# Kernel optimization log

Hardware: AMD Instinct MI355X
Metric: run time of the kernel (lower is better)

Reference implementation:

```python
import jax, jax.numpy as jnp
import numpy as np

N_NODES = 100000


def sage_conv(x, src, dst, W_l, b_l, W_r, n_nodes):
    # mean-aggregate source neighbors onto destination nodes (PyG SAGEConv, aggr='mean')
    agg = jax.ops.segment_sum(x[src], dst, num_segments=n_nodes)          # [N, d_in]
    cnt = jax.ops.segment_sum(jnp.ones((src.shape[0], 1), x.dtype), dst,
                              num_segments=n_nodes)                        # [N, 1]
    agg = agg / jnp.maximum(cnt, 1.0)  # isolated nodes -> 0, as in scatter-mean
    # out = lin_l(agg) + lin_r(x); bias lives in lin_l
    return agg @ W_l + b_l + x @ W_r


def setup_inputs() -> dict:
    key = jax.random.key(0)
    ks = jax.random.split(key, 12)
    d_in, h1, h2, h3 = 256, 256, 128, 1
    x = jax.random.normal(ks[0], (N_NODES, d_in), dtype=jnp.float32)
    edge_index = jax.random.randint(ks[1], (2, 1600000), 0, N_NODES, dtype=jnp.int64)

    def lin(k, din, dout):
        s = 1.0 / np.sqrt(din)
        return jax.random.uniform(k, (din, dout), jnp.float32, -s, s)

    return {
        "x": x,
        "edge_index": edge_index,
        "Wl1": lin(ks[2], d_in, h1), "bl1": jnp.zeros((h1,), jnp.float32), "Wr1": lin(ks[3], d_in, h1),
        "Wl2": lin(ks[4], h1, h2),  "bl2": jnp.zeros((h2,), jnp.float32), "Wr2": lin(ks[5], h1, h2),
        "Wl3": lin(ks[6], h2, h3),  "bl3": jnp.zeros((h3,), jnp.float32), "Wr3": lin(ks[7], h2, h3),
    }


def reference(x, edge_index, Wl1, bl1, Wr1, Wl2, bl2, Wr2, Wl3, bl3, Wr3):
    src, dst = edge_index[0], edge_index[1]
    n = x.shape[0]
    h = jax.nn.relu(sage_conv(x, src, dst, Wl1, bl1, Wr1, n))
    h = jax.nn.relu(sage_conv(h, src, dst, Wl2, bl2, Wr2, n))
    out = sage_conv(h, src, dst, Wl3, bl3, Wr3, n)
    return out  # [N, 1]
```

## Files before the change

kernel.cpp:

```cpp
#include <hip/hip_runtime.h>
#include <hip/hip_bf16.h>


typedef __attribute__((ext_vector_type(8))) short short8;
typedef __attribute__((ext_vector_type(4))) float f32x4;

__device__ __forceinline__ unsigned short f2b(float f) {
    __hip_bfloat16 h = __float2bfloat16(f);
    return *reinterpret_cast<unsigned short*>(&h);
}
__device__ __forceinline__ float b2f(unsigned short u) {
    union { unsigned int i; float f; } v; v.i = ((unsigned int)u) << 16; return v.f;
}
__device__ __forceinline__ unsigned char f2q(float f) {
    unsigned int p = __builtin_amdgcn_cvt_pk_fp8_f32(f, f, 0u, false);
    return (unsigned char)(p & 0xffu);
}

__device__ __forceinline__ void gload_lds16(const unsigned short* g, unsigned short* l) {
    __builtin_amdgcn_global_load_lds(
        (const __attribute__((address_space(1))) unsigned int*)(const void*)g,
        (__attribute__((address_space(3))) unsigned int*)(void*)l,
        16, 0, 0);
}

__device__ __forceinline__ void acc_fp8x8(const uint2 v, float* s) {
    s[0] += __builtin_amdgcn_cvt_f32_fp8(v.x, 0);
    s[1] += __builtin_amdgcn_cvt_f32_fp8(v.x, 1);
    s[2] += __builtin_amdgcn_cvt_f32_fp8(v.x, 2);
    s[3] += __builtin_amdgcn_cvt_f32_fp8(v.x, 3);
    s[4] += __builtin_amdgcn_cvt_f32_fp8(v.y, 0);
    s[5] += __builtin_amdgcn_cvt_f32_fp8(v.y, 1);
    s[6] += __builtin_amdgcn_cvt_f32_fp8(v.y, 2);
    s[7] += __builtin_amdgcn_cvt_f32_fp8(v.y, 3);
}

__global__ __launch_bounds__(256) void prep_fused(
    const float* __restrict__ x, unsigned short* __restrict__ xb,
    const float* __restrict__ Wl1, const float* __restrict__ Wr1,
    const float* __restrict__ Wl2, const float* __restrict__ Wr2,
    unsigned short* __restrict__ Wl1s, unsigned short* __restrict__ Wr1s,
    unsigned short* __restrict__ Wl2s, unsigned short* __restrict__ Wr2s,
    const int* __restrict__ dst, int* __restrict__ deg,
    unsigned short* __restrict__ rank, int E)
{
    const int b = blockIdx.x;
    const int tid = threadIdx.x;
    if (b < 25000) {
        const int i = b * 256 + tid;
        float4 v = *(const float4*)(x + (size_t)i * 4);
        ushort4 o;
        o.x = f2b(v.x); o.y = f2b(v.y); o.z = f2b(v.z); o.w = f2b(v.w);
        *(ushort4*)(xb + (size_t)i * 4) = o;
        if (tid < 64) {
            const int e = b * 64 + tid;
            if (e < E) rank[e] = (unsigned short)atomicAdd(&deg[dst[e]], 1);
        }
    } else {
        const float* W; unsigned short* O; int base, hs;
        if (b < 25256)      { W = Wl1; O = Wl1s; base = b - 25000; hs = 8; }
        else if (b < 25512) { W = Wr1; O = Wr1s; base = b - 25256; hs = 8; }
        else if (b < 25640) { W = Wl2; O = Wl2s; base = b - 25512; hs = 7; }
        else                { W = Wr2; O = Wr2s; base = b - 25640; hs = 7; }
        const int i = base * 256 + tid;
        const int k = i >> hs;
        const int h = i & ((1 << hs) - 1);
        O[((size_t)(((k >> 3) << hs) + h) << 3) + (k & 7)] = f2b(W[i]);
    }
}

__global__ __launch_bounds__(256) void scan_phaseA(int* __restrict__ a,
                                                   int* __restrict__ blockSums, int n) {
    __shared__ int sh[256];
    const int tid = threadIdx.x;
    const int base = blockIdx.x * 1024 + tid * 4;
    int v[4];
    #pragma unroll
    for (int i = 0; i < 4; ++i) v[i] = (base + i < n) ? a[base + i] : 0;
    int tsum = v[0] + v[1] + v[2] + v[3];
    sh[tid] = tsum;
    __syncthreads();
    for (int off = 1; off < 256; off <<= 1) {
        int t = (tid >= off) ? sh[tid - off] : 0;
        __syncthreads();
        sh[tid] += t;
        __syncthreads();
    }
    int run = sh[tid] - tsum;
    #pragma unroll
    for (int i = 0; i < 4; ++i) {
        if (base + i < n) a[base + i] = run;
        run += v[i];
    }
    if (tid == 255) blockSums[blockIdx.x] = sh[255];
}

__global__ __launch_bounds__(256) void scan_phaseB(int* __restrict__ bs, int nb) {
    __shared__ int sh[256];
    const int tid = threadIdx.x;
    int v = (tid < nb) ? bs[tid] : 0;
    sh[tid] = v;
    __syncthreads();
    for (int off = 1; off < 256; off <<= 1) {
        int t = (tid >= off) ? sh[tid - off] : 0;
        __syncthreads();
        sh[tid] += t;
        __syncthreads();
    }
    if (tid < nb) bs[tid] = sh[tid] - v;
}

__global__ __launch_bounds__(256) void scan_phaseC(int* __restrict__ a,
                                                   const int* __restrict__ bs, int n) {
    const int base = blockIdx.x * 1024 + threadIdx.x * 4;
    const int add = bs[blockIdx.x];
    #pragma unroll
    for (int i = 0; i < 4; ++i)
        if (base + i < n) a[base + i] += add;
}

__global__ __launch_bounds__(256) void gemm_l1_fill(
    const unsigned short* __restrict__ Xb,
    const unsigned short* __restrict__ Wsw_l,
    const unsigned short* __restrict__ Wsw_r,
    const float* __restrict__ bias,
    unsigned char* __restrict__ Tout,
    unsigned short* __restrict__ Abase,
    int M,
    const int* __restrict__ src, const int* __restrict__ dst,
    const int* __restrict__ starts, const unsigned short* __restrict__ rank,
    int* __restrict__ csr, int E)
{
    const int bid = (blockIdx.x & 7) * 1173 + (blockIdx.x >> 3);
    const int grp = bid / 3;
    const int rem = bid - grp * 3;
    const int tid = threadIdx.x;

    if (rem != 0) {
        const int e = (grp * 2 + rem - 1) * 256 + tid;
        if (e < E) csr[starts[dst[e]] + (int)rank[e]] = src[e];
        return;
    }

    __shared__ unsigned short smem[16384];

    const int wid = tid >> 6;
    const int lane = tid & 63;
    const int quad = lane >> 4;
    const int l15 = lane & 15;
    const int col0 = (grp & 3) << 6;
    const int m0 = (grp >> 2) * 128;

    const unsigned short* aSrc[4];
    unsigned int aOfs[4];
    #pragma unroll
    for (int i = 0; i < 4; ++i) {
        const int slot = i * 256 + tid;
        const int r = slot >> 3, cs = slot & 7;
        const int cg = cs ^ (r & 7);
        aSrc[i] = Xb + ((size_t)(m0 + r) << 8) + (cg << 3);
        aOfs[i] = (unsigned)((i * 256 + wid * 64) * 8);
    }
    const unsigned short* bSrc[4];
    unsigned int bOfs[4];
    #pragma unroll
    for (int i = 0; i < 4; ++i) {
        const int slot = i * 256 + tid;
        const int mat = slot >> 9, ko = (slot >> 6) & 7, col = slot & 63;
        const unsigned short* Wm = mat ? Wsw_r : Wsw_l;
        bSrc[i] = Wm + (((size_t)ko * 256 + col0 + col) << 3);
        bOfs[i] = (unsigned)(8192 + (i * 256 + wid * 64) * 8);
    }

    const f32x4 zero = {0.f, 0.f, 0.f, 0.f};
    f32x4 acc[2][8];
    #pragma unroll
    for (int mt = 0; mt < 2; ++mt)
        #pragma unroll
        for (int nt = 0; nt < 8; ++nt) acc[mt][nt] = zero;

    for (int ks = 0; ks < 4; ++ks) {
        #pragma unroll
        for (int i = 0; i < 4; ++i)
            gload_lds16(aSrc[i] + ks * 64, smem + aOfs[i]);
        #pragma unroll
        for (int i = 0; i < 4; ++i)
            gload_lds16(bSrc[i] + ks * 16384, smem + bOfs[i]);
        __syncthreads();

        #pragma unroll
        for (int k32 = 0; k32 < 2; ++k32) {
            short8 af[2], bf[8];
            #pragma unroll
            for (int mt = 0; mt < 2; ++mt) {
                const int row = wid * 32 + mt * 16 + l15;
                const int c = (k32 * 4 + quad) ^ (row & 7);
                af[mt] = *(const short8*)(smem + ((row << 3) + c) * 8);
            }
            #pragma unroll
            for (int nt = 0; nt < 4; ++nt) {
                const int colL = nt * 16 + l15;
                const int ko = k32 * 4 + quad;
                bf[nt]     = *(const short8*)(smem + 8192 + ((ko << 6) + colL) * 8);
                bf[nt + 4] = *(const short8*)(smem + 8192 + (512 + (ko << 6) + colL) * 8);
            }
            #pragma unroll
            for (int mt = 0; mt < 2; ++mt)
                #pragma unroll
                for (int nt = 0; nt < 8; ++nt)
                    acc[mt][nt] = __builtin_amdgcn_mfma_f32_16x16x32_bf16(
                        af[mt], bf[nt], acc[mt][nt], 0, 0, 0);
        }
        __syncthreads();
    }

    #pragma unroll
    for (int nt = 0; nt < 4; ++nt) {
        const int colg = col0 + nt * 16 + l15;
        const float bb = bias[colg];
        #pragma unroll
        for (int mt = 0; mt < 2; ++mt) {
            const int gmb = m0 + wid * 32 + mt * 16 + quad * 4;
            #pragma unroll
            for (int r = 0; r < 4; ++r) {
                if (gmb + r < M) {
                    Tout [(size_t)(gmb + r) * 256 + colg] = f2q(acc[mt][nt][r]);
                    Abase[(size_t)(gmb + r) * 256 + colg] = f2b(acc[mt][nt + 4][r] + bb);
                }
            }
        }
    }
}

__global__ __launch_bounds__(256) void agg256_b(
    const int* __restrict__ endoff, const int* __restrict__ csr,
    const unsigned char* __restrict__ T,
    const unsigned short* __restrict__ Abase, unsigned short* __restrict__ Xout,
    int N, int E)
{
    const int node = (int)((blockIdx.x * 256 + threadIdx.x) >> 5);
    const int lane = threadIdx.x & 31;
    const int hsel = threadIdx.x & 32;
    if (node >= N) return;
    const int beg = endoff[node];
    const int end = (node + 1 < N) ? endoff[node + 1] : E;
    float s[8] = {0.f, 0.f, 0.f, 0.f, 0.f, 0.f, 0.f, 0.f};

    for (int base = beg; base < end; base += 32) {
        const int il = base + lane;
        const int vidx = csr[il < E ? il : (E - 1)];
        const int cnt = (end - base < 32) ? (end - base) : 32;
        int u = 0;
        for (; u + 16 <= cnt; u += 16) {
            uint2 v[16];
            #pragma unroll
            for (int k = 0; k < 16; ++k) {
                const int r = __shfl(vidx, (u + k) | hsel, 64);
                v[k] = *(const uint2*)(T + ((size_t)r << 8) + (lane << 3));
            }
            #pragma unroll
            for (int k = 0; k < 16; ++k) acc_fp8x8(v[k], s);
        }
        if (u + 8 <= cnt) {
            uint2 v[8];
            #pragma unroll
            for (int k = 0; k < 8; ++k) {
                const int r = __shfl(vidx, (u + k) | hsel, 64);
                v[k] = *(const uint2*)(T + ((size_t)r << 8) + (lane << 3));
            }
            #pragma unroll
            for (int k = 0; k < 8; ++k) acc_fp8x8(v[k], s);
            u += 8;
        }
        for (; u < cnt; ++u) {
            const int r = __shfl(vidx, u | hsel, 64);
            const uint2 v = *(const uint2*)(T + ((size_t)r << 8) + (lane << 3));
            acc_fp8x8(v, s);
        }
    }

    const float w = 1.0f / fmaxf((float)(end - beg), 1.0f);
    const short8 bu = *(const short8*)(Abase + ((size_t)node << 8) + (lane << 3));
    short8 o;
    #pragma unroll
    for (int j = 0; j < 8; ++j)
        o[j] = (short)f2b(fmaxf(b2f((unsigned short)bu[j]) + s[j] * w, 0.f));
    *(short8*)(Xout + ((size_t)node << 8) + (lane << 3)) = o;
}

__global__ __launch_bounds__(256) void gemm_bf16(
    const unsigned short* __restrict__ Xb,
    const unsigned short* __restrict__ Wsw_l,
    const unsigned short* __restrict__ Wsw_r,
    const float* __restrict__ bias,
    unsigned char* __restrict__ Tout,
    unsigned short* __restrict__ Abase,
    int M, int H)
{
    const int tid = threadIdx.x;
    const int wid = tid >> 6;
    const int lane = tid & 63;
    const int quad = lane >> 4;
    const int l15 = lane & 15;

    const int col0 = blockIdx.x << 6;
    const int m0 = blockIdx.y * 128 + wid * 32;

    const unsigned short* aptr[2];
    #pragma unroll
    for (int mt = 0; mt < 2; ++mt) {
        int r = m0 + mt * 16 + l15;
        if (r > M - 1) r = M - 1;
        aptr[mt] = Xb + ((size_t)r << 8) + (quad << 3);
    }
    const unsigned short* bptr[8];
    #pragma unroll
    for (int nt = 0; nt < 4; ++nt) {
        const int col = col0 + nt * 16 + l15;
        bptr[nt]     = Wsw_l + (((size_t)quad * H + col) << 3);
        bptr[nt + 4] = Wsw_r + (((size_t)quad * H + col) << 3);
    }

    const f32x4 zero = {0.f, 0.f, 0.f, 0.f};
    f32x4 acc[2][8];
    #pragma unroll
    for (int mt = 0; mt < 2; ++mt)
        #pragma unroll
        for (int nt = 0; nt < 8; ++nt) acc[mt][nt] = zero;

    #pragma unroll 2
    for (int ks = 0; ks < 8; ++ks) {
        short8 af[2], bf[8];
        #pragma unroll
        for (int mt = 0; mt < 2; ++mt)
            af[mt] = *(const short8*)(aptr[mt] + ks * 32);
        #pragma unroll
        for (int nt = 0; nt < 8; ++nt)
            bf[nt] = *(const short8*)(bptr[nt] + (size_t)ks * 32 * H);
        #pragma unroll
        for (int mt = 0; mt < 2; ++mt)
            #pragma unroll
            for (int nt = 0; nt < 8; ++nt)
                acc[mt][nt] = __builtin_amdgcn_mfma_f32_16x16x32_bf16(
                    af[mt], bf[nt], acc[mt][nt], 0, 0, 0);
    }

    #pragma unroll
    for (int nt = 0; nt < 4; ++nt) {
        const int colg = col0 + nt * 16 + l15;
        const float bb = bias[colg];
        #pragma unroll
        for (int mt = 0; mt < 2; ++mt) {
            const int gmb = m0 + mt * 16 + quad * 4;
            #pragma unroll
            for (int r = 0; r < 4; ++r) {
                if (gmb + r < M) {
                    Tout [(size_t)(gmb + r) * H + colg] = f2q(acc[mt][nt][r]);
                    Abase[(size_t)(gmb + r) * H + colg] = f2b(acc[mt][nt + 4][r] + bb);
                }
            }
        }
    }
}

__global__ __launch_bounds__(256) void agg_gemv3(
    const int* __restrict__ endoff, const int* __restrict__ csr,
    const unsigned char* __restrict__ T,
    const unsigned short* __restrict__ Ab,
    const float* __restrict__ Wl, const float* __restrict__ Wr,
    const float* __restrict__ b,
    float* __restrict__ t3, float* __restrict__ out, int N, int E)
{
    const int node = (int)((blockIdx.x * 256 + threadIdx.x) >> 5);
    const int lane = threadIdx.x & 31;
    const int hsel = threadIdx.x & 32;
    if (node >= N) return;
    const int beg = endoff[node];
    const int end = (node + 1 < N) ? endoff[node + 1] : E;
    float s0 = 0.f, s1 = 0.f, s2 = 0.f, s3 = 0.f;

    for (int base = beg; base < end; base += 32) {
        const int il = base + lane;
        const int vidx = csr[il < E ? il : (E - 1)];
        const int cnt = (end - base < 32) ? (end - base) : 32;
        int u = 0;
        for (; u + 16 <= cnt; u += 16) {
            unsigned int v[16];
            #pragma unroll
            for (int k = 0; k < 16; ++k) {
                const int r = __shfl(vidx, (u + k) | hsel, 64);
                v[k] = *(const unsigned int*)(T + ((size_t)r << 7) + (lane << 2));
            }
            #pragma unroll
            for (int k = 0; k < 16; ++k) {
                s0 += __builtin_amdgcn_cvt_f32_fp8(v[k], 0);
                s1 += __builtin_amdgcn_cvt_f32_fp8(v[k], 1);
                s2 += __builtin_amdgcn_cvt_f32_fp8(v[k], 2);
                s3 += __builtin_amdgcn_cvt_f32_fp8(v[k], 3);
            }
        }
        if (u + 8 <= cnt) {
            unsigned int v[8];
            #pragma unroll
            for (int k = 0; k < 8; ++k) {
                const int r = __shfl(vidx, (u + k) | hsel, 64);
                v[k] = *(const unsigned int*)(T + ((size_t)r << 7) + (lane << 2));
            }
            #pragma unroll
            for (int k = 0; k < 8; ++k) {
                s0 += __builtin_amdgcn_cvt_f32_fp8(v[k], 0);
                s1 += __builtin_amdgcn_cvt_f32_fp8(v[k], 1);
                s2 += __builtin_amdgcn_cvt_f32_fp8(v[k], 2);
                s3 += __builtin_amdgcn_cvt_f32_fp8(v[k], 3);
            }
            u += 8;
        }
        for (; u < cnt; ++u) {
            const int r = __shfl(vidx, u | hsel, 64);
            const unsigned int v = *(const unsigned int*)(T + ((size_t)r << 7) + (lane << 2));
            s0 += __builtin_amdgcn_cvt_f32_fp8(v, 0);
            s1 += __builtin_amdgcn_cvt_f32_fp8(v, 1);
            s2 += __builtin_amdgcn_cvt_f32_fp8(v, 2);
            s3 += __builtin_amdgcn_cvt_f32_fp8(v, 3);
        }
    }

    const float w = 1.0f / fmaxf((float)(end - beg), 1.0f);
    const ushort4 bu = *(const ushort4*)(Ab + ((size_t)node << 7) + (lane << 2));
    const float h0 = fmaxf(b2f(bu.x) + s0 * w, 0.f);
    const float h1 = fmaxf(b2f(bu.y) + s1 * w, 0.f);
    const float h2 = fmaxf(b2f(bu.z) + s2 * w, 0.f);
    const float h3 = fmaxf(b2f(bu.w) + s3 * w, 0.f);

    const float4 wl = *(const float4*)(Wl + (lane << 2));
    const float4 wr = *(const float4*)(Wr + (lane << 2));
    float dl = h0 * wl.x + h1 * wl.y + h2 * wl.z + h3 * wl.w;
    float dr = h0 * wr.x + h1 * wr.y + h2 * wr.z + h3 * wr.w;
    #pragma unroll
    for (int off = 16; off > 0; off >>= 1) {
        dl += __shfl_down(dl, off, 64);
        dr += __shfl_down(dr, off, 64);
    }
    if (lane == 0) {
        t3[node] = dl;
        out[node] = dr + b[0];
    }
}

__global__ __launch_bounds__(256) void agg1(
    const int* __restrict__ endoff, const int* __restrict__ csr,
    const float* __restrict__ t3, float* __restrict__ out, int N, int E)
{
    const int i = blockIdx.x * blockDim.x + threadIdx.x;
    if (i >= N) return;
    const int beg = endoff[i];
    const int end = (i + 1 < N) ? endoff[i + 1] : E;
    int p = beg;
    float s = 0.f;
    for (; p + 4 <= end; p += 4)
        s += (t3[csr[p]] + t3[csr[p + 1]]) + (t3[csr[p + 2]] + t3[csr[p + 3]]);
    for (; p < end; ++p) s += t3[csr[p]];
    out[i] += s / fmaxf((float)(end - beg), 1.0f);
}

extern "C" void kernel_launch(void* const* d_in, const int* in_sizes, int n_in,
                              void* d_out, int out_size, void* d_ws, size_t ws_size,
                              hipStream_t stream) {
    const float* x   = (const float*)d_in[0];
    const int*   ei  = (const int*)d_in[1];
    const float* Wl1 = (const float*)d_in[2];
    const float* bl1 = (const float*)d_in[3];
    const float* Wr1 = (const float*)d_in[4];
    const float* Wl2 = (const float*)d_in[5];
    const float* bl2 = (const float*)d_in[6];
    const float* Wr2 = (const float*)d_in[7];
    const float* Wl3 = (const float*)d_in[8];
    const float* bl3 = (const float*)d_in[9];
    const float* Wr3 = (const float*)d_in[10];
    float* out = (float*)d_out;

    const int N = in_sizes[0] / 256;
    const int E = in_sizes[1] / 2;
    const int* src = ei;
    const int* dst = ei + E;

    char* W = (char*)d_ws;
    const size_t MB512 = (size_t)100000 * 512;
    unsigned short* X1b = (unsigned short*)(W);
    unsigned char*  T1b = (unsigned char*)(W + MB512);
    unsigned short* A1b = (unsigned short*)(W + 2 * MB512);
    unsigned short* X2b = (unsigned short*)(W);
    unsigned char*  T2b = (unsigned char*)(W + MB512);
    unsigned short* A2b = (unsigned short*)(W + MB512 + MB512 / 2);
    char* S = W + 3 * MB512;
    int*   endoff = (int*)(S);
    int*   bsums  = (int*)(S + (size_t)N * 4);
    float* t3     = (float*)(S + (size_t)N * 4 + 1024);
    int*   csr    = (int*)(S + (size_t)N * 8 + 1024);
    unsigned short* Wl1s = (unsigned short*)(S + (size_t)N * 8 + 1024 + (size_t)E * 4);
    unsigned short* Wr1s = Wl1s + 65536;
    unsigned short* Wl2s = Wr1s + 65536;
    unsigned short* Wr2s = Wl2s + 32768;
    unsigned short* rank = Wr2s + 32768;

    hipMemsetAsync(endoff, 0, (size_t)N * sizeof(int), stream);
    prep_fused<<<25768, 256, 0, stream>>>(
        x, X1b, Wl1, Wr1, Wl2, Wr2, Wl1s, Wr1s, Wl2s, Wr2s,
        dst, endoff, rank, E);
    const int nScanBlocks = (N + 1023) / 1024;
    scan_phaseA<<<nScanBlocks, 256, 0, stream>>>(endoff, bsums, N);
    scan_phaseB<<<1, 256, 0, stream>>>(bsums, nScanBlocks);
    scan_phaseC<<<nScanBlocks, 256, 0, stream>>>(endoff, bsums, N);

    gemm_l1_fill<<<3128 * 3, 256, 0, stream>>>(X1b, Wl1s, Wr1s, bl1, T1b, A1b, N,
                                               src, dst, endoff, rank, csr, E);

    agg256_b<<<(N * 32 + 255) / 256, 256, 0, stream>>>(endoff, csr, T1b, A1b, X2b, N, E);
    gemm_bf16<<<dim3(2, (N + 127) / 128), 256, 0, stream>>>(X2b, Wl2s, Wr2s, bl2,
                                                            T2b, A2b, N, 128);

    agg_gemv3<<<(N * 32 + 255) / 256, 256, 0, stream>>>(endoff, csr, T2b, A2b,
                                                        Wl3, Wr3, bl3, t3, out, N, E);
    agg1<<<(N + 255) / 256, 256, 0, stream>>>(endoff, csr, t3, out, N, E);
}
```

Baseline: 482.1 us.

## Store layer-1 fp8 transform in column-sliced layout and aggregate per slice

The layer-1 GEMM now writes the fp8 transformed features as 8 column slices of 32 bytes per node, each slice contiguous over nodes. The aggregation kernel becomes agg256_s: each block handles one slice, and 4 lanes cover a node's 32-byte slice, so 16 nodes share a wave. The aim is a smaller per-slice gather working set that fits cache better. The cost is that each edge index is reread 8 times, and the per-node loop with one index per step gives less memory-level parallelism than the old shuffle-batched gathers.

```diff
diff --git a/kernel.cpp b/kernel.cpp
--- a/kernel.cpp
+++ b/kernel.cpp
@@ -218,13 +218,14 @@
     for (int nt = 0; nt < 4; ++nt) {
         const int colg = col0 + nt * 16 + l15;
         const float bb = bias[colg];
+        const size_t sbase = (size_t)(colg >> 5) * (size_t)M * 32 + (colg & 31);
         #pragma unroll
         for (int mt = 0; mt < 2; ++mt) {
             const int gmb = m0 + wid * 32 + mt * 16 + quad * 4;
             #pragma unroll
             for (int r = 0; r < 4; ++r) {
                 if (gmb + r < M) {
-                    Tout [(size_t)(gmb + r) * 256 + colg] = f2q(acc[mt][nt][r]);
+                    Tout [sbase + (size_t)(gmb + r) * 32] = f2q(acc[mt][nt][r]);
                     Abase[(size_t)(gmb + r) * 256 + colg] = f2b(acc[mt][nt + 4][r] + bb);
                 }
             }
@@ -232,60 +233,45 @@
     }
 }
 
-__global__ __launch_bounds__(256) void agg256_b(
+__global__ __launch_bounds__(256) void agg256_s(
     const int* __restrict__ endoff, const int* __restrict__ csr,
     const unsigned char* __restrict__ T,
     const unsigned short* __restrict__ Abase, unsigned short* __restrict__ Xout,
     int N, int E)
 {
-    const int node = (int)((blockIdx.x * 256 + threadIdx.x) >> 5);
-    const int lane = threadIdx.x & 31;
-    const int hsel = threadIdx.x & 32;
+    const int slice = blockIdx.x & 7;
+    const int lane  = threadIdx.x & 63;
+    const int g     = lane >> 2;
+    const int boff  = lane & 3;
+    const int node  = (blockIdx.x >> 3) * 64 + (threadIdx.x >> 6) * 16 + g;
     if (node >= N) return;
     const int beg = endoff[node];
     const int end = (node + 1 < N) ? endoff[node + 1] : E;
+    const unsigned char* Ts = T + (size_t)slice * (size_t)N * 32 + (boff << 3);
+
     float s[8] = {0.f, 0.f, 0.f, 0.f, 0.f, 0.f, 0.f, 0.f};
-
-    for (int base = beg; base < end; base += 32) {
-        const int il = base + lane;
-        const int vidx = csr[il < E ? il : (E - 1)];
-        const int cnt = (end - base < 32) ? (end - base) : 32;
-        int u = 0;
-        for (; u + 16 <= cnt; u += 16) {
-            uint2 v[16];
-            #pragma unroll
-            for (int k = 0; k < 16; ++k) {
-                const int r = __shfl(vidx, (u + k) | hsel, 64);
-                v[k] = *(const uint2*)(T + ((size_t)r << 8) + (lane << 3));
-            }
-            #pragma unroll
-            for (int k = 0; k < 16; ++k) acc_fp8x8(v[k], s);
-        }
-        if (u + 8 <= cnt) {
-            uint2 v[8];
-            #pragma unroll
-            for (int k = 0; k < 8; ++k) {
-                const int r = __shfl(vidx, (u + k) | hsel, 64);
-                v[k] = *(const uint2*)(T + ((size_t)r << 8) + (lane << 3));
-            }
-            #pragma unroll
-            for (int k = 0; k < 8; ++k) acc_fp8x8(v[k], s);
-            u += 8;
-        }
-        for (; u < cnt; ++u) {
-            const int r = __shfl(vidx, u | hsel, 64);
-            const uint2 v = *(const uint2*)(T + ((size_t)r << 8) + (lane << 3));
-            acc_fp8x8(v, s);
-        }
+    int p = beg;
+    for (; p + 4 <= end; p += 4) {
+        const int r0 = csr[p], r1 = csr[p + 1], r2 = csr[p + 2], r3 = csr[p + 3];
+        const uint2 v0 = *(const uint2*)(Ts + ((size_t)r0 << 5));
+        const uint2 v1 = *(const uint2*)(Ts + ((size_t)r1 << 5));
+        const uint2 v2 = *(const uint2*)(Ts + ((size_t)r2 << 5));
+        const uint2 v3 = *(const uint2*)(Ts + ((size_t)r3 << 5));
+        acc_fp8x8(v0, s); acc_fp8x8(v1, s); acc_fp8x8(v2, s); acc_fp8x8(v3, s);
+    }
+    for (; p < end; ++p) {
+        const uint2 v = *(const uint2*)(Ts + ((size_t)csr[p] << 5));
+        acc_fp8x8(v, s);
     }
 
     const float w = 1.0f / fmaxf((float)(end - beg), 1.0f);
-    const short8 bu = *(const short8*)(Abase + ((size_t)node << 8) + (lane << 3));
+    const size_t doff = (size_t)node * 256 + (slice << 5) + (boff << 3);
+    const short8 bu = *(const short8*)(Abase + doff);
     short8 o;
     #pragma unroll
     for (int j = 0; j < 8; ++j)
         o[j] = (short)f2b(fmaxf(b2f((unsigned short)bu[j]) + s[j] * w, 0.f));
-    *(short8*)(Xout + ((size_t)node << 8) + (lane << 3)) = o;
+    *(short8*)(Xout + doff) = o;
 }
 
 __global__ __launch_bounds__(256) void gemm_bf16(
@@ -515,7 +501,7 @@
     gemm_l1_fill<<<3128 * 3, 256, 0, stream>>>(X1b, Wl1s, Wr1s, bl1, T1b, A1b, N,
                                                src, dst, endoff, rank, csr, E);
 
-    agg256_b<<<(N * 32 + 255) / 256, 256, 0, stream>>>(endoff, csr, T1b, A1b, X2b, N, E);
+    agg256_s<<<((N + 63) / 64) * 8, 256, 0, stream>>>(endoff, csr, T1b, A1b, X2b, N, E);
     gemm_bf16<<<dim3(2, (N + 127) / 128), 256, 0, stream>>>(X2b, Wl2s, Wr2s, bl2,
                                                             T2b, A2b, N, 128);
 
```

Result: slower. 502.8 us (+4.3%).
